# Performance work log

Hardware: AMD Instinct MI355X
Metric: run time of the kernel (lower is better)

The kernel has to match this reference:

```python
import jax, jax.numpy as jnp
import numpy as np

N = 20480    # total nodes in batched graph (64 graphs x 320 nodes)
E = 327680   # edges, avg in-degree 16
G = 64       # graphs in the batch
IN_DIM = 128
H = 4        # attention heads per layer
D = 64       # hidden dim per head (num_hidden)
C = 10       # num_classes
NEG_SLOPE = 0.2


def _gat_layer(h, src, dst, W, al, ar, residual):
    # DGL GATConv: fc -> per-head attention logits -> edge softmax over dst -> scatter-sum
    z = (h @ W).reshape(N, H, D)                       # [N,H,D]
    el = jnp.sum(z * al, axis=-1)                      # [N,H]
    er = jnp.sum(z * ar, axis=-1)                      # [N,H]
    e = jax.nn.leaky_relu(el[src] + er[dst], NEG_SLOPE)  # [E,H]
    m = jax.lax.stop_gradient(jax.ops.segment_max(e, dst, num_segments=N))
    m = jnp.where(jnp.isfinite(m), m, 0.0)
    ex = jnp.exp(e - m[dst])                           # [E,H]
    s = jax.ops.segment_sum(ex, dst, num_segments=N)   # [N,H]
    a = ex / jnp.where(s > 0, s, 1.0)[dst]             # [E,H] edge softmax
    msg = z[src] * a[:, :, None]                       # [E,H,D] (dominant intermediate)
    out = jax.ops.segment_sum(msg, dst, num_segments=N)  # [N,H,D]
    if residual:
        out = out + h.reshape(N, H, D)                 # res_fc is Identity (in == H*D)
        out = jax.nn.elu(out)                          # GATConv-internal activation
    return jax.nn.elu(out.reshape(N, H * D))           # model-level activation after flatten


def setup_inputs() -> dict:
    key = jax.random.key(0)
    ks = jax.random.split(key, 16)
    x = jax.random.normal(ks[0], (N, IN_DIM), jnp.float32)
    src = jax.random.randint(ks[1], (E,), 0, N, dtype=jnp.int32)
    # guarantee every node has >= 1 incoming edge (valid softmax denominator)
    dst = jnp.concatenate([jnp.arange(N, dtype=jnp.int32),
                           jax.random.randint(ks[2], (E - N,), 0, N, dtype=jnp.int32)])
    graph_ids = jnp.repeat(jnp.arange(G, dtype=jnp.int32), N // G)

    def lin(k, fi, fo):
        return (jax.random.normal(k, (fi, fo), jnp.float32) / np.float32(np.sqrt(fi)))

    def attn(k):
        return jax.random.normal(k, (H, D), jnp.float32) * np.float32(0.1)

    return {
        "x": x, "src": src, "dst": dst, "graph_ids": graph_ids,
        "W0": lin(ks[3], IN_DIM, H * D), "al0": attn(ks[4]), "ar0": attn(ks[5]),
        "W1": lin(ks[6], H * D, H * D), "al1": attn(ks[7]), "ar1": attn(ks[8]),
        "W2": lin(ks[9], H * D, H * D), "al2": attn(ks[10]), "ar2": attn(ks[11]),
        "Wc": lin(ks[12], H * D, C),
        "bc": jnp.zeros((C,), jnp.float32),
    }


def reference(x, src, dst, graph_ids, W0, al0, ar0, W1, al1, ar1, W2, al2, ar2, Wc, bc):
    h = _gat_layer(x, src, dst, W0, al0, ar0, residual=False)  # layer 0: no residual/act inside
    h = _gat_layer(h, src, dst, W1, al1, ar1, residual=True)
    h = _gat_layer(h, src, dst, W2, al2, ar2, residual=True)
    # dgl.mean_nodes: per-graph mean over node features
    hg = jax.ops.segment_sum(h, graph_ids, num_segments=G) / np.float32(N // G)  # [G, H*D]
    hg = jax.nn.elu(hg)
    return hg @ Wc + bc                                        # [G, C] logits
```

## Files before the change

### kernel.cpp

```cpp
#include <hip/hip_runtime.h>


#define NNODES 20480
#define NEDGES 327680
#define NGRAPH 64
#define NPG    320
#define HD     256
#define NH     4
#define NCLS   10

typedef __attribute__((ext_vector_type(8))) short short8;
typedef __attribute__((ext_vector_type(4))) float f32x4;

__device__ __forceinline__ float elu_f(float x)   { return x > 0.f ? x : expm1f(x); }
__device__ __forceinline__ float lrelu_f(float x) { return x > 0.f ? x : 0.2f * x; }

__device__ __forceinline__ ushort f2bf(float v) {
    uint u = __float_as_uint(v);
    uint r = (u + 0x7fffu + ((u >> 16) & 1u)) >> 16;
    return (ushort)r;
}
__device__ __forceinline__ float bf2f(ushort u) {
    return __uint_as_float(((uint)u) << 16);
}

__global__ void zero_i32(int* p, int n) {
    int i = blockIdx.x * blockDim.x + threadIdx.x;
    if (i < n) p[i] = 0;
}

__global__ void count_k(const int* __restrict__ dst, int* __restrict__ counts) {
    int e = blockIdx.x * blockDim.x + threadIdx.x;
    if (e < NEDGES) atomicAdd(&counts[dst[e]], 1);
}

__global__ void scan_k(const int* __restrict__ counts, int* __restrict__ row_ptr,
                       int* __restrict__ cursor) {
    __shared__ int sm[1024];
    int t = threadIdx.x;
    const int CH = NNODES / 1024;
    int base = t * CH;
    int s = 0;
    for (int j = 0; j < CH; j++) s += counts[base + j];
    sm[t] = s;
    __syncthreads();
    for (int off = 1; off < 1024; off <<= 1) {
        int v = (t >= off) ? sm[t - off] : 0;
        __syncthreads();
        sm[t] += v;
        __syncthreads();
    }
    int run = sm[t] - s;
    if (t == 0) row_ptr[0] = 0;
    for (int j = 0; j < CH; j++) {
        cursor[base + j] = run;
        run += counts[base + j];
        row_ptr[base + 1 + j] = run;
    }
}

__global__ void fill_k(const int* __restrict__ src, const int* __restrict__ dst,
                       int* __restrict__ cursor, int* __restrict__ edge_src) {
    int e = blockIdx.x * blockDim.x + threadIdx.x;
    if (e < NEDGES) {
        int d = dst[e];
        int pos = atomicAdd(&cursor[d], 1);
        edge_src[pos] = src[e];
    }
}

__global__ void xsplit_k(const float* __restrict__ x, ushort* __restrict__ hi,
                         ushort* __restrict__ lo) {
    int i = blockIdx.x * 256 + threadIdx.x;
    float v = x[i];
    ushort h = f2bf(v);
    hi[i] = h;
    lo[i] = f2bf(v - bf2f(h));
}

__global__ void wsplit_k(const float* __restrict__ W0, ushort* __restrict__ B0h, ushort* __restrict__ B0l,
                         const float* __restrict__ W1, ushort* __restrict__ B1h, ushort* __restrict__ B1l,
                         const float* __restrict__ W2, ushort* __restrict__ B2h, ushort* __restrict__ B2l) {
    int idx = blockIdx.x * 256 + threadIdx.x;
    const float* W; ushort *Bh, *Bl;
    if (idx < 128 * 256)          { W = W0; Bh = B0h; Bl = B0l; }
    else if (idx < 384 * 256)     { W = W1; Bh = B1h; Bl = B1l; idx -= 128 * 256; }
    else                          { W = W2; Bh = B2h; Bl = B2l; idx -= 384 * 256; }
    int k = idx >> 8, col = idx & 255;
    float v = W[idx];
    ushort h = f2bf(v);
    float vh = bf2f(h);
    ushort l = f2bf(v - vh);
    size_t o = (size_t)(k >> 5) * 8192 + (size_t)col * 32 + (k & 31);
    Bh[o] = h;
    Bl[o] = l;
}

__global__ __launch_bounds__(256) void gemm_mfma_k(
        const ushort* __restrict__ Ahi, const ushort* __restrict__ Alo,
        const ushort* __restrict__ Bhi, const ushort* __restrict__ Blo,
        const float* __restrict__ al_, const float* __restrict__ ar_,
        ushort* __restrict__ zbf, float* __restrict__ el, float* __restrict__ er,
        int K) {
    int m0 = blockIdx.x * 32;
    int w = threadIdx.x >> 6, l = threadIdx.x & 63;
    int n0 = w * 64;
    int lr = l & 15, lk = l >> 4;
    f32x4 acc[2][4] = {};
    int ksteps = K >> 5;
    for (int kt = 0; kt < ksteps; kt++) {
        int kbase = kt * 32 + lk * 8;
        short8 a_hi[2], a_lo[2], b_hi[4], b_lo[4];
        #pragma unroll
        for (int i = 0; i < 2; i++) {
            size_t off = (size_t)(m0 + i * 16 + lr) * K + kbase;
            a_hi[i] = *reinterpret_cast<const short8*>(Ahi + off);
            a_lo[i] = *reinterpret_cast<const short8*>(Alo + off);
        }
        #pragma unroll
        for (int j = 0; j < 4; j++) {
            size_t off = (size_t)kt * 8192 + (size_t)(n0 + j * 16 + lr) * 32 + lk * 8;
            b_hi[j] = *reinterpret_cast<const short8*>(Bhi + off);
            b_lo[j] = *reinterpret_cast<const short8*>(Blo + off);
        }
        #pragma unroll
        for (int i = 0; i < 2; i++)
            #pragma unroll
            for (int j = 0; j < 4; j++) {
                acc[i][j] = __builtin_amdgcn_mfma_f32_16x16x32_bf16(a_hi[i], b_hi[j], acc[i][j], 0, 0, 0);
                acc[i][j] = __builtin_amdgcn_mfma_f32_16x16x32_bf16(a_hi[i], b_lo[j], acc[i][j], 0, 0, 0);
                acc[i][j] = __builtin_amdgcn_mfma_f32_16x16x32_bf16(a_lo[i], b_hi[j], acc[i][j], 0, 0, 0);
            }
    }
    float alv[4], arv[4];
    #pragma unroll
    for (int j = 0; j < 4; j++) {
        int col = n0 + j * 16 + lr;
        alv[j] = al_[col];
        arv[j] = ar_[col];
    }
    #pragma unroll
    for (int i = 0; i < 2; i++) {
        #pragma unroll
        for (int r = 0; r < 4; r++) {
            float pel = 0.f, per = 0.f;
            #pragma unroll
            for (int j = 0; j < 4; j++) {
                float v = acc[i][j][r];
                pel += v * alv[j];
                per += v * arv[j];
                int row = m0 + i * 16 + lk * 4 + r;
                int col = n0 + j * 16 + lr;
                zbf[(size_t)row * HD + col] = f2bf(v);
            }
            #pragma unroll
            for (int off = 1; off < 16; off <<= 1) {
                pel += __shfl_xor(pel, off);
                per += __shfl_xor(per, off);
            }
            if (lr == 0) {
                int row = m0 + i * 16 + lk * 4 + r;
                el[row * NH + w] = pel;
                er[row * NH + w] = per;
            }
        }
    }
}

__global__ __launch_bounds__(256) void attn_aggr_k(
        const ushort* __restrict__ zbf,
        const float* __restrict__ el, const float* __restrict__ er,
        const int* __restrict__ row_ptr, const int* __restrict__ edge_src,
        const float* __restrict__ hin, float* __restrict__ hout,
        ushort* __restrict__ hhi, ushort* __restrict__ hlo,
        int residual, int write_split) {
    int wid = threadIdx.x >> 6, lane = threadIdx.x & 63;
    int n = blockIdx.x * 4 + wid;
    int h = lane >> 4, j16 = lane & 15;
    int hbase = lane & 48;
    int col = j16 * 4 + h * 64;
    int beg = row_ptr[n], end = row_ptr[n + 1];
    int deg = end - beg;
    float ern = er[n * NH + h];
    float4 acc = make_float4(0.f, 0.f, 0.f, 0.f);

    if (deg <= 64) {
        float pv[4];
        int   sv[4];
        #pragma unroll
        for (int u = 0; u < 4; u++) {
            int k = beg + u * 16 + j16;
            if (k < end) {
                sv[u] = edge_src[k];
                pv[u] = lrelu_f(el[sv[u] * NH + h] + ern);
            } else {
                sv[u] = 0;
                pv[u] = -3.4e38f;
            }
        }
        float m = fmaxf(fmaxf(pv[0], pv[1]), fmaxf(pv[2], pv[3]));
        #pragma unroll
        for (int off = 1; off < 16; off <<= 1) m = fmaxf(m, __shfl_xor(m, off));
        float ssum = 0.f;
        #pragma unroll
        for (int u = 0; u < 4; u++) {
            int k = beg + u * 16 + j16;
            pv[u] = (k < end) ? __expf(pv[u] - m) : 0.f;
            ssum += pv[u];
        }
        #pragma unroll
        for (int off = 1; off < 16; off <<= 1) ssum += __shfl_xor(ssum, off);
        float rinv = 1.f / ssum;
        #pragma unroll
        for (int u = 0; u < 4; u++) pv[u] *= rinv;
        #pragma unroll
        for (int u = 0; u < 4; u++) {
            int kb = beg + u * 16;
            if (kb >= end) break;
            int cnt = end - kb;
            if (cnt > 16) cnt = 16;
            for (int j = 0; j < cnt; j++) {
                float w = __shfl(pv[u], hbase + j);
                int   s = __shfl(sv[u], hbase + j);
                ushort4 zv = *reinterpret_cast<const ushort4*>(&zbf[(size_t)s * HD + col]);
                acc.x += bf2f(zv.x) * w;
                acc.y += bf2f(zv.y) * w;
                acc.z += bf2f(zv.z) * w;
                acc.w += bf2f(zv.w) * w;
            }
        }
    } else {
        float m = -3.4e38f;
        for (int k = beg + j16; k < end; k += 16)
            m = fmaxf(m, lrelu_f(el[edge_src[k] * NH + h] + ern));
        #pragma unroll
        for (int off = 1; off < 16; off <<= 1) m = fmaxf(m, __shfl_xor(m, off));
        float ssum = 0.f;
        for (int k = beg + j16; k < end; k += 16)
            ssum += __expf(lrelu_f(el[edge_src[k] * NH + h] + ern) - m);
        #pragma unroll
        for (int off = 1; off < 16; off <<= 1) ssum += __shfl_xor(ssum, off);
        float rinv = 1.f / ssum;
        for (int k = beg; k < end; k++) {
            int s = edge_src[k];
            float w = __expf(lrelu_f(el[s * NH + h] + ern) - m) * rinv;
            ushort4 zv = *reinterpret_cast<const ushort4*>(&zbf[(size_t)s * HD + col]);
            acc.x += bf2f(zv.x) * w;
            acc.y += bf2f(zv.y) * w;
            acc.z += bf2f(zv.z) * w;
            acc.w += bf2f(zv.w) * w;
        }
    }

    size_t o = (size_t)n * HD + col;
    float4 r;
    if (residual) {
        float4 hv = *reinterpret_cast<const float4*>(&hin[o]);
        r.x = elu_f(elu_f(acc.x + hv.x));
        r.y = elu_f(elu_f(acc.y + hv.y));
        r.z = elu_f(elu_f(acc.z + hv.z));
        r.w = elu_f(elu_f(acc.w + hv.w));
    } else {
        r.x = elu_f(acc.x);
        r.y = elu_f(acc.y);
        r.z = elu_f(acc.z);
        r.w = elu_f(acc.w);
    }
    *reinterpret_cast<float4*>(&hout[o]) = r;
    if (write_split) {
        ushort4 uh, ul;
        uh.x = f2bf(r.x); ul.x = f2bf(r.x - bf2f(uh.x));
        uh.y = f2bf(r.y); ul.y = f2bf(r.y - bf2f(uh.y));
        uh.z = f2bf(r.z); ul.z = f2bf(r.z - bf2f(uh.z));
        uh.w = f2bf(r.w); ul.w = f2bf(r.w - bf2f(uh.w));
        *reinterpret_cast<ushort4*>(&hhi[o]) = uh;
        *reinterpret_cast<ushort4*>(&hlo[o]) = ul;
    }
}

__global__ __launch_bounds__(256) void pool_k(const float* __restrict__ h,
                                              float* __restrict__ hg) {
    int g = blockIdx.x, t = threadIdx.x;
    const float* p = h + (size_t)g * NPG * HD + t;
    float s = 0.f;
    for (int i = 0; i < NPG; i++) s += p[(size_t)i * HD];
    s *= (1.0f / NPG);
    hg[g * HD + t] = elu_f(s);
}

__global__ void cls_k(const float* __restrict__ hg, const float* __restrict__ Wc,
                      const float* __restrict__ bc, float* __restrict__ out) {
    int g = blockIdx.x, c = threadIdx.x;
    if (c < NCLS) {
        float s = bc[c];
        for (int k = 0; k < HD; k++) s += hg[g * HD + k] * Wc[k * NCLS + c];
        out[g * NCLS + c] = s;
    }
}

extern "C" void kernel_launch(void* const* d_in, const int* in_sizes, int n_in,
                              void* d_out, int out_size, void* d_ws, size_t ws_size,
                              hipStream_t stream) {
    const float* x   = (const float*)d_in[0];
    const int*   src = (const int*)d_in[1];
    const int*   dst = (const int*)d_in[2];
    const float* W0  = (const float*)d_in[4];
    const float* al0 = (const float*)d_in[5];
    const float* ar0 = (const float*)d_in[6];
    const float* W1  = (const float*)d_in[7];
    const float* al1 = (const float*)d_in[8];
    const float* ar1 = (const float*)d_in[9];
    const float* W2  = (const float*)d_in[10];
    const float* al2 = (const float*)d_in[11];
    const float* ar2 = (const float*)d_in[12];
    const float* Wc  = (const float*)d_in[13];
    const float* bc  = (const float*)d_in[14];
    float* out = (float*)d_out;

    char* ws = (char*)d_ws;
    size_t off = 0;
    auto alloc = [&](size_t bytes) -> void* {
        void* p = ws + off;
        off = (off + bytes + 255) & ~(size_t)255;
        return p;
    };
    float*  hbuf     = (float*)alloc((size_t)NNODES * HD * 4);
    ushort* zbf      = (ushort*)alloc((size_t)NNODES * HD * 2);
    float*  el       = (float*)alloc((size_t)NNODES * NH * 4);
    float*  er       = (float*)alloc((size_t)NNODES * NH * 4);
    int*    counts   = (int*)alloc((size_t)NNODES * 4);
    int*    row_ptr  = (int*)alloc((size_t)(NNODES + 1) * 4);
    int*    cursor   = (int*)alloc((size_t)NNODES * 4);
    int*    edge_src = (int*)alloc((size_t)NEDGES * 4);
    float*  hg       = (float*)alloc((size_t)NGRAPH * HD * 4);
    ushort* xhi      = (ushort*)alloc((size_t)NNODES * 128 * 2);
    ushort* xlo      = (ushort*)alloc((size_t)NNODES * 128 * 2);
    ushort* hhi      = (ushort*)alloc((size_t)NNODES * HD * 2);
    ushort* hlo      = (ushort*)alloc((size_t)NNODES * HD * 2);
    ushort* B0h      = (ushort*)alloc((size_t)128 * 256 * 2);
    ushort* B0l      = (ushort*)alloc((size_t)128 * 256 * 2);
    ushort* B1h      = (ushort*)alloc((size_t)256 * 256 * 2);
    ushort* B1l      = (ushort*)alloc((size_t)256 * 256 * 2);
    ushort* B2h      = (ushort*)alloc((size_t)256 * 256 * 2);
    ushort* B2l      = (ushort*)alloc((size_t)256 * 256 * 2);

    zero_i32<<<NNODES / 256, 256, 0, stream>>>(counts, NNODES);
    count_k<<<NEDGES / 256, 256, 0, stream>>>(dst, counts);
    scan_k<<<1, 1024, 0, stream>>>(counts, row_ptr, cursor);
    fill_k<<<NEDGES / 256, 256, 0, stream>>>(src, dst, cursor, edge_src);

    xsplit_k<<<NNODES * 128 / 256, 256, 0, stream>>>(x, xhi, xlo);
    wsplit_k<<<(128 + 256 + 256) * 256 / 256, 256, 0, stream>>>(
        W0, B0h, B0l, W1, B1h, B1l, W2, B2h, B2l);

    auto layer = [&](const ushort* Ah, const ushort* Al, const ushort* Bh,
                     const ushort* Bl, const float* al_, const float* ar_,
                     const float* hin, float* hout, int K, int residual, int wsplit) {
        gemm_mfma_k<<<NNODES / 32, 256, 0, stream>>>(Ah, Al, Bh, Bl, al_, ar_,
                                                     zbf, el, er, K);
        attn_aggr_k<<<NNODES / 4, 256, 0, stream>>>(zbf, el, er, row_ptr, edge_src,
                                                    hin, hout, hhi, hlo,
                                                    residual, wsplit);
    };

    layer(xhi, xlo, B0h, B0l, al0, ar0, nullptr, hbuf, 128, 0, 1);
    layer(hhi, hlo, B1h, B1l, al1, ar1, hbuf, hbuf, 256, 1, 1);
    layer(hhi, hlo, B2h, B2l, al2, ar2, hbuf, hbuf, 256, 1, 0);

    pool_k<<<NGRAPH, 256, 0, stream>>>(hbuf, hg);
    cls_k<<<NGRAPH, 64, 0, stream>>>(hg, Wc, bc, out);
}
```

Before: 338.8 us.

## Split fp32 activations to bf16 hi/lo inside GEMM and fuse pool with classifier

```diff
diff --git a/kernel.cpp b/kernel.cpp
--- a/kernel.cpp
+++ b/kernel.cpp
@@ -24,9 +24,19 @@
     return __uint_as_float(((uint)u) << 16);
 }
 
-__global__ void zero_i32(int* p, int n) {
-    int i = blockIdx.x * blockDim.x + threadIdx.x;
-    if (i < n) p[i] = 0;
+__device__ __forceinline__ void split8(const float* __restrict__ p,
+                                       short8& hi, short8& lo) {
+    float4 a = *reinterpret_cast<const float4*>(p);
+    float4 b = *reinterpret_cast<const float4*>(p + 4);
+    float v[8] = {a.x, a.y, a.z, a.w, b.x, b.y, b.z, b.w};
+    #pragma unroll
+    for (int e = 0; e < 8; e++) {
+        uint u = __float_as_uint(v[e]);
+        hi[e] = (short)(u >> 16);
+        float hf = __uint_as_float(u & 0xFFFF0000u);
+        float lf = v[e] - hf;
+        lo[e] = (short)(__float_as_uint(lf) >> 16);
+    }
 }
 
 __global__ void count_k(const int* __restrict__ dst, int* __restrict__ counts) {
@@ -67,15 +77,6 @@
         int pos = atomicAdd(&cursor[d], 1);
         edge_src[pos] = src[e];
     }
-}
-
-__global__ void xsplit_k(const float* __restrict__ x, ushort* __restrict__ hi,
-                         ushort* __restrict__ lo) {
-    int i = blockIdx.x * 256 + threadIdx.x;
-    float v = x[i];
-    ushort h = f2bf(v);
-    hi[i] = h;
-    lo[i] = f2bf(v - bf2f(h));
 }
 
 __global__ void wsplit_k(const float* __restrict__ W0, ushort* __restrict__ B0h, ushort* __restrict__ B0l,
@@ -97,7 +98,7 @@
 }
 
 __global__ __launch_bounds__(256) void gemm_mfma_k(
-        const ushort* __restrict__ Ahi, const ushort* __restrict__ Alo,
+        const float* __restrict__ A,
         const ushort* __restrict__ Bhi, const ushort* __restrict__ Blo,
         const float* __restrict__ al_, const float* __restrict__ ar_,
         ushort* __restrict__ zbf, float* __restrict__ el, float* __restrict__ er,
@@ -114,8 +115,7 @@
         #pragma unroll
         for (int i = 0; i < 2; i++) {
             size_t off = (size_t)(m0 + i * 16 + lr) * K + kbase;
-            a_hi[i] = *reinterpret_cast<const short8*>(Ahi + off);
-            a_lo[i] = *reinterpret_cast<const short8*>(Alo + off);
+            split8(A + off, a_hi[i], a_lo[i]);
         }
         #pragma unroll
         for (int j = 0; j < 4; j++) {
@@ -172,8 +172,7 @@
         const float* __restrict__ el, const float* __restrict__ er,
         const int* __restrict__ row_ptr, const int* __restrict__ edge_src,
         const float* __restrict__ hin, float* __restrict__ hout,
-        ushort* __restrict__ hhi, ushort* __restrict__ hlo,
-        int residual, int write_split) {
+        int residual) {
     int wid = threadIdx.x >> 6, lane = threadIdx.x & 63;
     int n = blockIdx.x * 4 + wid;
     int h = lane >> 4, j16 = lane & 15;
@@ -216,17 +215,28 @@
         #pragma unroll
         for (int u = 0; u < 4; u++) {
             int kb = beg + u * 16;
-            if (kb >= end) break;
-            int cnt = end - kb;
-            if (cnt > 16) cnt = 16;
-            for (int j = 0; j < cnt; j++) {
-                float w = __shfl(pv[u], hbase + j);
-                int   s = __shfl(sv[u], hbase + j);
-                ushort4 zv = *reinterpret_cast<const ushort4*>(&zbf[(size_t)s * HD + col]);
-                acc.x += bf2f(zv.x) * w;
-                acc.y += bf2f(zv.y) * w;
-                acc.z += bf2f(zv.z) * w;
-                acc.w += bf2f(zv.w) * w;
+            if (kb + 16 <= end) {
+                #pragma unroll
+                for (int j = 0; j < 16; j++) {
+                    float w = __shfl(pv[u], hbase + j);
+                    int   s = __shfl(sv[u], hbase + j);
+                    ushort4 zv = *reinterpret_cast<const ushort4*>(&zbf[(size_t)s * HD + col]);
+                    acc.x += bf2f(zv.x) * w;
+                    acc.y += bf2f(zv.y) * w;
+                    acc.z += bf2f(zv.z) * w;
+                    acc.w += bf2f(zv.w) * w;
+                }
+            } else if (kb < end) {
+                int cnt = end - kb;
+                for (int j = 0; j < cnt; j++) {
+                    float w = __shfl(pv[u], hbase + j);
+                    int   s = __shfl(sv[u], hbase + j);
+                    ushort4 zv = *reinterpret_cast<const ushort4*>(&zbf[(size_t)s * HD + col]);
+                    acc.x += bf2f(zv.x) * w;
+                    acc.y += bf2f(zv.y) * w;
+                    acc.z += bf2f(zv.z) * w;
+                    acc.w += bf2f(zv.w) * w;
+                }
             }
         }
     } else {
@@ -267,34 +277,23 @@
         r.w = elu_f(acc.w);
     }
     *reinterpret_cast<float4*>(&hout[o]) = r;
-    if (write_split) {
-        ushort4 uh, ul;
-        uh.x = f2bf(r.x); ul.x = f2bf(r.x - bf2f(uh.x));
-        uh.y = f2bf(r.y); ul.y = f2bf(r.y - bf2f(uh.y));
-        uh.z = f2bf(r.z); ul.z = f2bf(r.z - bf2f(uh.z));
-        uh.w = f2bf(r.w); ul.w = f2bf(r.w - bf2f(uh.w));
-        *reinterpret_cast<ushort4*>(&hhi[o]) = uh;
-        *reinterpret_cast<ushort4*>(&hlo[o]) = ul;
-    }
-}
-
-__global__ __launch_bounds__(256) void pool_k(const float* __restrict__ h,
-                                              float* __restrict__ hg) {
+}
+
+__global__ __launch_bounds__(256) void poolcls_k(const float* __restrict__ h,
+                                                 const float* __restrict__ Wc,
+                                                 const float* __restrict__ bc,
+                                                 float* __restrict__ out) {
+    __shared__ float sh[HD];
     int g = blockIdx.x, t = threadIdx.x;
     const float* p = h + (size_t)g * NPG * HD + t;
     float s = 0.f;
     for (int i = 0; i < NPG; i++) s += p[(size_t)i * HD];
-    s *= (1.0f / NPG);
-    hg[g * HD + t] = elu_f(s);
-}
-
-__global__ void cls_k(const float* __restrict__ hg, const float* __restrict__ Wc,
-                      const float* __restrict__ bc, float* __restrict__ out) {
-    int g = blockIdx.x, c = threadIdx.x;
-    if (c < NCLS) {
-        float s = bc[c];
-        for (int k = 0; k < HD; k++) s += hg[g * HD + k] * Wc[k * NCLS + c];
-        out[g * NCLS + c] = s;
+    sh[t] = elu_f(s * (1.0f / NPG));
+    __syncthreads();
+    if (t < NCLS) {
+        float acc = bc[t];
+        for (int k = 0; k < HD; k++) acc += sh[k] * Wc[k * NCLS + t];
+        out[g * NCLS + t] = acc;
     }
 }
 
@@ -332,11 +331,6 @@
     int*    row_ptr  = (int*)alloc((size_t)(NNODES + 1) * 4);
     int*    cursor   = (int*)alloc((size_t)NNODES * 4);
     int*    edge_src = (int*)alloc((size_t)NEDGES * 4);
-    float*  hg       = (float*)alloc((size_t)NGRAPH * HD * 4);
-    ushort* xhi      = (ushort*)alloc((size_t)NNODES * 128 * 2);
-    ushort* xlo      = (ushort*)alloc((size_t)NNODES * 128 * 2);
-    ushort* hhi      = (ushort*)alloc((size_t)NNODES * HD * 2);
-    ushort* hlo      = (ushort*)alloc((size_t)NNODES * HD * 2);
     ushort* B0h      = (ushort*)alloc((size_t)128 * 256 * 2);
     ushort* B0l      = (ushort*)alloc((size_t)128 * 256 * 2);
     ushort* B1h      = (ushort*)alloc((size_t)256 * 256 * 2);
@@ -344,29 +338,26 @@
     ushort* B2h      = (ushort*)alloc((size_t)256 * 256 * 2);
     ushort* B2l      = (ushort*)alloc((size_t)256 * 256 * 2);
 
-    zero_i32<<<NNODES / 256, 256, 0, stream>>>(counts, NNODES);
+    hipMemsetAsync(counts, 0, (size_t)NNODES * 4, stream);
     count_k<<<NEDGES / 256, 256, 0, stream>>>(dst, counts);
     scan_k<<<1, 1024, 0, stream>>>(counts, row_ptr, cursor);
     fill_k<<<NEDGES / 256, 256, 0, stream>>>(src, dst, cursor, edge_src);
 
-    xsplit_k<<<NNODES * 128 / 256, 256, 0, stream>>>(x, xhi, xlo);
     wsplit_k<<<(128 + 256 + 256) * 256 / 256, 256, 0, stream>>>(
         W0, B0h, B0l, W1, B1h, B1l, W2, B2h, B2l);
 
-    auto layer = [&](const ushort* Ah, const ushort* Al, const ushort* Bh,
-                     const ushort* Bl, const float* al_, const float* ar_,
-                     const float* hin, float* hout, int K, int residual, int wsplit) {
-        gemm_mfma_k<<<NNODES / 32, 256, 0, stream>>>(Ah, Al, Bh, Bl, al_, ar_,
+    auto layer = [&](const float* A, const ushort* Bh, const ushort* Bl,
+                     const float* al_, const float* ar_,
+                     const float* hin, float* hout, int K, int residual) {
+        gemm_mfma_k<<<NNODES / 32, 256, 0, stream>>>(A, Bh, Bl, al_, ar_,
                                                      zbf, el, er, K);
         attn_aggr_k<<<NNODES / 4, 256, 0, stream>>>(zbf, el, er, row_ptr, edge_src,
-                                                    hin, hout, hhi, hlo,
-                                                    residual, wsplit);
+                                                    hin, hout, residual);
     };
 
-    layer(xhi, xlo, B0h, B0l, al0, ar0, nullptr, hbuf, 128, 0, 1);
-    layer(hhi, hlo, B1h, B1l, al1, ar1, hbuf, hbuf, 256, 1, 1);
-    layer(hhi, hlo, B2h, B2l, al2, ar2, hbuf, hbuf, 256, 1, 0);
-
-    pool_k<<<NGRAPH, 256, 0, stream>>>(hbuf, hg);
-    cls_k<<<NGRAPH, 64, 0, stream>>>(hg, Wc, bc, out);
-}
+    layer(x,    B0h, B0l, al0, ar0, nullptr, hbuf, 128, 0);
+    layer(hbuf, B1h, B1l, al1, ar1, hbuf, hbuf, 256, 1);
+    layer(hbuf, B2h, B2l, al2, ar2, hbuf, hbuf, 256, 1);
+
+    poolcls_k<<<NGRAPH, 256, 0, stream>>>(hbuf, Wc, bc, out);
+}
```

New measurement: 314.7 us. -7.1%, faster.
